# Kernel tuning notes

Measured on AMD Instinct MI355X. Metric: run time of the kernel, lower is better.

The kernel has to match this reference:

```python
import jax, jax.numpy as jnp
import numpy as np

N_NODES = 100000
N_EDGES = 640000
H = 128


def setup_inputs() -> dict:
    key = jax.random.key(0)
    ks = jax.random.split(key, 6)
    s = 1.0 / np.sqrt(H)
    x = jax.random.normal(ks[0], (N_NODES, H), dtype=jnp.float32)
    src = jax.random.randint(ks[1], (N_EDGES,), 0, N_NODES, dtype=jnp.int64)
    dst = jax.random.randint(ks[2], (N_EDGES,), 0, N_NODES, dtype=jnp.int64)
    W1 = jax.random.normal(ks[3], (H, H), dtype=jnp.float32) * s
    W2 = jax.random.normal(ks[4], (H, H), dtype=jnp.float32) * s
    W3 = jax.random.normal(ks[5], (H, 1), dtype=jnp.float32) * s
    return {
        "x": x, "src": src, "dst": dst,
        "W1": W1, "b1": jnp.zeros((H,), jnp.float32),
        "W2": W2, "b2": jnp.zeros((H,), jnp.float32),
        "W3": W3, "b3": jnp.zeros((1,), jnp.float32),
    }


def reference(x, src, dst, W1, b1, W2, b2, W3, b3):
    # per-edge gather of src/dst node feats, elementwise product: [E, H]
    h = x[src] * x[dst]
    # 3-layer MLP (Linear-ReLU-Linear-ReLU-Linear) per edge -> [E, 1]
    h = jax.nn.relu(h @ W1 + b1)
    h = jax.nn.relu(h @ W2 + b2)
    return h @ W3 + b3
```

## Files before the change

### kernel.cpp

```cpp
#include <hip/hip_runtime.h>
#include <hip/hip_bf16.h>

#define HDIM 128

typedef short bf16x8 __attribute__((ext_vector_type(8)));
typedef float f32x4 __attribute__((ext_vector_type(4)));

__device__ __forceinline__ short f2bf(float f) {
    __hip_bfloat16 h = __float2bfloat16(f);
    return __builtin_bit_cast(short, h);
}

__device__ __forceinline__ float bf2f(short s) {
    unsigned u = ((unsigned)(unsigned short)s) << 16;
    return __builtin_bit_cast(float, u);
}

__device__ __forceinline__ bf16x8 ldB(const short* sW, int n, int chunk) {
    return *(const bf16x8*)(sW + n * HDIM + ((chunk ^ (n & 7)) << 3));
}

__device__ __forceinline__ bf16x8 gatherA_f32(const float* xs, const float* xd, int k0) {
    float4 a0 = *(const float4*)(xs + k0);
    float4 a1 = *(const float4*)(xs + k0 + 4);
    float4 c0 = *(const float4*)(xd + k0);
    float4 c1 = *(const float4*)(xd + k0 + 4);
    bf16x8 r = { f2bf(a0.x * c0.x), f2bf(a0.y * c0.y), f2bf(a0.z * c0.z), f2bf(a0.w * c0.w),
                 f2bf(a1.x * c1.x), f2bf(a1.y * c1.y), f2bf(a1.z * c1.z), f2bf(a1.w * c1.w) };
    return r;
}

__global__ void cvt_kernel(const float* __restrict__ x, unsigned short* __restrict__ xb, int n4) {
    int i = blockIdx.x * blockDim.x + threadIdx.x;
    const int stride = gridDim.x * blockDim.x;
    for (; i < n4; i += stride) {
        float4 v = ((const float4*)x)[i];
        ushort4 o;
        o.x = (unsigned short)f2bf(v.x);
        o.y = (unsigned short)f2bf(v.y);
        o.z = (unsigned short)f2bf(v.z);
        o.w = (unsigned short)f2bf(v.w);
        ((ushort4*)xb)[i] = o;
    }
}

template<bool XBF>
__global__ __launch_bounds__(256, 2)
void edge_mlp_kernel(const float* __restrict__ x,
                     const unsigned short* __restrict__ xb,
                     const int* __restrict__ src,
                     const int* __restrict__ dst,
                     const float* __restrict__ W1, const float* __restrict__ b1,
                     const float* __restrict__ W2, const float* __restrict__ b2,
                     const float* __restrict__ W3, const float* __restrict__ b3,
                     float* __restrict__ out, int E, int ntiles)
{
    __shared__ short sW1[HDIM * HDIM];
    __shared__ short sW2[HDIM * HDIM];
    __shared__ short sH1[4][32 * 64];

    const int tid = threadIdx.x;

    {
        const int n  = tid & 127;
        const int kh = tid >> 7;
        for (int c = 0; c < 8; ++c) {
            const int kc = kh * 8 + c;
            const int k0 = kc * 8;
            short v1[8], v2[8];
            #pragma unroll
            for (int j = 0; j < 8; ++j) {
                v1[j] = f2bf(W1[(k0 + j) * HDIM + n]);
                v2[j] = f2bf(W2[(k0 + j) * HDIM + n]);
            }
            const int off = n * HDIM + ((kc ^ (n & 7)) << 3);
            bf16x8 t1 = { v1[0], v1[1], v1[2], v1[3], v1[4], v1[5], v1[6], v1[7] };
            bf16x8 t2 = { v2[0], v2[1], v2[2], v2[3], v2[4], v2[5], v2[6], v2[7] };
            *(bf16x8*)(sW1 + off) = t1;
            *(bf16x8*)(sW2 + off) = t2;
        }
    }
    __syncthreads();

    const int w    = tid >> 6;
    const int lane = tid & 63;
    const int g    = lane >> 4;
    const int e16  = lane & 15;
    short* myH1 = &sH1[w][0];

    float b1v[8], b2v[8], w3v[8];
    #pragma unroll
    for (int nt = 0; nt < 8; ++nt) {
        b1v[nt] = b1[nt * 16 + e16];
        b2v[nt] = b2[nt * 16 + e16];
        w3v[nt] = W3[nt * 16 + e16];
    }
    const float b3s = b3[0];

    if (blockIdx.x >= ntiles) return;

    int tile = blockIdx.x;
    int s0, d0, s1, d1;
    {
        const int base = (tile << 7) + (w << 5);
        int a0 = base + e16;       a0 = a0 < E ? a0 : 0;
        int a1 = base + 16 + e16;  a1 = a1 < E ? a1 : 0;
        s0 = src[a0]; d0 = dst[a0]; s1 = src[a1]; d1 = dst[a1];
    }
    bf16x8 rS0[4], rD0[4], rS1[4], rD1[4];
    if constexpr (XBF) {
        const unsigned short* pxs0 = xb + (size_t)s0 * HDIM;
        const unsigned short* pxd0 = xb + (size_t)d0 * HDIM;
        const unsigned short* pxs1 = xb + (size_t)s1 * HDIM;
        const unsigned short* pxd1 = xb + (size_t)d1 * HDIM;
        #pragma unroll
        for (int t = 0; t < 4; ++t) {
            const int k0 = t * 32 + g * 8;
            rS0[t] = *(const bf16x8*)(pxs0 + k0);
            rD0[t] = *(const bf16x8*)(pxd0 + k0);
            rS1[t] = *(const bf16x8*)(pxs1 + k0);
            rD1[t] = *(const bf16x8*)(pxd1 + k0);
        }
    }

    for (;;) {
        const int nxt = tile + gridDim.x;
        const bool hasNext = nxt < ntiles;

        int ns0, nd0, ns1, nd1;
        {
            const int nb = hasNext ? (nxt << 7) + (w << 5) : 0;
            int a0 = nb + e16;       a0 = a0 < E ? a0 : 0;
            int a1 = nb + 16 + e16;  a1 = a1 < E ? a1 : 0;
            ns0 = src[a0]; nd0 = dst[a0]; ns1 = src[a1]; nd1 = dst[a1];
        }

        const int base = (tile << 7) + (w << 5);

        f32x4 acc[2][8];
        #pragma unroll
        for (int nt = 0; nt < 8; ++nt) {
            f32x4 iv = { b1v[nt], b1v[nt], b1v[nt], b1v[nt] };
            acc[0][nt] = iv;
            acc[1][nt] = iv;
        }

        if constexpr (XBF) {
            #pragma unroll
            for (int t = 0; t < 4; ++t) {
                bf16x8 a0, a1;
                #pragma unroll
                for (int j = 0; j < 8; ++j) {
                    a0[j] = f2bf(bf2f(rS0[t][j]) * bf2f(rD0[t][j]));
                    a1[j] = f2bf(bf2f(rS1[t][j]) * bf2f(rD1[t][j]));
                }
                #pragma unroll
                for (int nt = 0; nt < 8; ++nt) {
                    bf16x8 bb = ldB(sW1, nt * 16 + e16, t * 4 + g);
                    acc[0][nt] = __builtin_amdgcn_mfma_f32_16x16x32_bf16(a0, bb, acc[0][nt], 0, 0, 0);
                    acc[1][nt] = __builtin_amdgcn_mfma_f32_16x16x32_bf16(a1, bb, acc[1][nt], 0, 0, 0);
                }
            }
        } else {
            const float* xs0 = x + (size_t)s0 * HDIM;
            const float* xd0 = x + (size_t)d0 * HDIM;
            const float* xs1 = x + (size_t)s1 * HDIM;
            const float* xd1 = x + (size_t)d1 * HDIM;
            #pragma unroll
            for (int t = 0; t < 4; ++t) {
                const int k0 = t * 32 + g * 8;
                bf16x8 a0 = gatherA_f32(xs0, xd0, k0);
                bf16x8 a1 = gatherA_f32(xs1, xd1, k0);
                #pragma unroll
                for (int nt = 0; nt < 8; ++nt) {
                    bf16x8 bb = ldB(sW1, nt * 16 + e16, t * 4 + g);
                    acc[0][nt] = __builtin_amdgcn_mfma_f32_16x16x32_bf16(a0, bb, acc[0][nt], 0, 0, 0);
                    acc[1][nt] = __builtin_amdgcn_mfma_f32_16x16x32_bf16(a1, bb, acc[1][nt], 0, 0, 0);
                }
            }
        }

        bf16x8 nS0[4], nD0[4], nS1[4], nD1[4];
        if constexpr (XBF) {
            const unsigned short* pxs0 = xb + (size_t)ns0 * HDIM;
            const unsigned short* pxd0 = xb + (size_t)nd0 * HDIM;
            const unsigned short* pxs1 = xb + (size_t)ns1 * HDIM;
            const unsigned short* pxd1 = xb + (size_t)nd1 * HDIM;
            #pragma unroll
            for (int t = 0; t < 4; ++t) {
                const int k0 = t * 32 + g * 8;
                nS0[t] = *(const bf16x8*)(pxs0 + k0);
                nD0[t] = *(const bf16x8*)(pxd0 + k0);
                nS1[t] = *(const bf16x8*)(pxs1 + k0);
                nD1[t] = *(const bf16x8*)(pxd1 + k0);
            }
        }

        f32x4 acc2[2][8];
        #pragma unroll
        for (int nt = 0; nt < 8; ++nt) {
            f32x4 iv = { b2v[nt], b2v[nt], b2v[nt], b2v[nt] };
            acc2[0][nt] = iv;
            acc2[1][nt] = iv;
        }
        #pragma unroll
        for (int khf = 0; khf < 2; ++khf) {
            #pragma unroll
            for (int ntl = 0; ntl < 4; ++ntl) {
                const int nt = khf * 4 + ntl;
                #pragma unroll
                for (int mt = 0; mt < 2; ++mt) {
                    #pragma unroll
                    for (int r = 0; r < 4; ++r) {
                        const int e  = mt * 16 + g * 4 + r;
                        const int kk = ntl * 16 + e16;
                        float v = acc[mt][nt][r];
                        v = v > 0.0f ? v : 0.0f;
                        myH1[e * 64 + (((kk >> 3) ^ (e & 7)) << 3) + (kk & 7)] = f2bf(v);
                    }
                }
            }
            #pragma unroll
            for (int tl = 0; tl < 2; ++tl) {
                const int ck = tl * 4 + g;
                bf16x8 a0 = *(const bf16x8*)(myH1 + e16 * 64 + ((ck ^ (e16 & 7)) << 3));
                bf16x8 a1 = *(const bf16x8*)(myH1 + (e16 + 16) * 64 + ((ck ^ ((e16 + 16) & 7)) << 3));
                const int t2 = khf * 2 + tl;
                #pragma unroll
                for (int nt = 0; nt < 8; ++nt) {
                    bf16x8 bb = ldB(sW2, nt * 16 + e16, t2 * 4 + g);
                    acc2[0][nt] = __builtin_amdgcn_mfma_f32_16x16x32_bf16(a0, bb, acc2[0][nt], 0, 0, 0);
                    acc2[1][nt] = __builtin_amdgcn_mfma_f32_16x16x32_bf16(a1, bb, acc2[1][nt], 0, 0, 0);
                }
            }
        }

        #pragma unroll
        for (int mt = 0; mt < 2; ++mt) {
            float p0 = 0.f, p1 = 0.f, p2 = 0.f, p3 = 0.f;
            #pragma unroll
            for (int nt = 0; nt < 8; ++nt) {
                f32x4 v = acc2[mt][nt];
                float r0 = v[0] > 0.f ? v[0] : 0.f;
                float r1 = v[1] > 0.f ? v[1] : 0.f;
                float r2 = v[2] > 0.f ? v[2] : 0.f;
                float r3 = v[3] > 0.f ? v[3] : 0.f;
                p0 += r0 * w3v[nt];
                p1 += r1 * w3v[nt];
                p2 += r2 * w3v[nt];
                p3 += r3 * w3v[nt];
            }
            #pragma unroll
            for (int off = 1; off < 16; off <<= 1) {
                p0 += __shfl_xor(p0, off);
                p1 += __shfl_xor(p1, off);
                p2 += __shfl_xor(p2, off);
                p3 += __shfl_xor(p3, off);
            }
            if (e16 == 0) {
                const int eb = base + mt * 16 + g * 4;
                if (eb + 0 < E) out[eb + 0] = p0 + b3s;
                if (eb + 1 < E) out[eb + 1] = p1 + b3s;
                if (eb + 2 < E) out[eb + 2] = p2 + b3s;
                if (eb + 3 < E) out[eb + 3] = p3 + b3s;
            }
        }

        if (!hasNext) break;
        tile = nxt;
        s0 = ns0; d0 = nd0; s1 = ns1; d1 = nd1;
        if constexpr (XBF) {
            #pragma unroll
            for (int t = 0; t < 4; ++t) {
                rS0[t] = nS0[t]; rD0[t] = nD0[t];
                rS1[t] = nS1[t]; rD1[t] = nD1[t];
            }
        }
    }
}

extern "C" void kernel_launch(void* const* d_in, const int* in_sizes, int n_in,
                              void* d_out, int out_size, void* d_ws, size_t ws_size,
                              hipStream_t stream) {
    const float* x   = (const float*)d_in[0];
    const int*   src = (const int*)d_in[1];
    const int*   dst = (const int*)d_in[2];
    const float* W1  = (const float*)d_in[3];
    const float* b1  = (const float*)d_in[4];
    const float* W2  = (const float*)d_in[5];
    const float* b2  = (const float*)d_in[6];
    const float* W3  = (const float*)d_in[7];
    const float* b3  = (const float*)d_in[8];
    float* out = (float*)d_out;

    const int xelems = in_sizes[0];
    const int E = in_sizes[1];
    const int ntiles = (E + 127) >> 7;
    const int grid = ntiles < 512 ? ntiles : 512;

    const size_t need = (size_t)xelems * sizeof(unsigned short);
    if (ws_size >= need) {
        unsigned short* xb = (unsigned short*)d_ws;
        const int n4 = xelems >> 2;
        hipLaunchKernelGGL(cvt_kernel, dim3(2048), dim3(256), 0, stream, x, xb, n4);
        hipLaunchKernelGGL((edge_mlp_kernel<true>), dim3(grid), dim3(256), 0, stream,
                           x, xb, src, dst, W1, b1, W2, b2, W3, b3, out, E, ntiles);
    } else {
        hipLaunchKernelGGL((edge_mlp_kernel<false>), dim3(grid), dim3(256), 0, stream,
                           x, (const unsigned short*)nullptr, src, dst,
                           W1, b1, W2, b2, W3, b3, out, E, ntiles);
    }
}
```

Measured before the change: 91.43 us.

## Bucket-sort edges by source node block to improve gather locality

```diff
diff --git a/kernel.cpp b/kernel.cpp
--- a/kernel.cpp
+++ b/kernel.cpp
@@ -2,6 +2,7 @@
 #include <hip/hip_bf16.h>
 
 #define HDIM 128
+#define NB   1024
 
 typedef short bf16x8 __attribute__((ext_vector_type(8)));
 typedef float f32x4 __attribute__((ext_vector_type(4)));
@@ -44,12 +45,53 @@
     }
 }
 
-template<bool XBF>
+__global__ void hist_kernel(const int* __restrict__ src, int* __restrict__ hist, int E) {
+    __shared__ int h[NB];
+    for (int i = threadIdx.x; i < NB; i += blockDim.x) h[i] = 0;
+    __syncthreads();
+    int i = blockIdx.x * blockDim.x + threadIdx.x;
+    for (; i < E; i += gridDim.x * blockDim.x) atomicAdd(&h[src[i] >> 7], 1);
+    __syncthreads();
+    for (int i2 = threadIdx.x; i2 < NB; i2 += blockDim.x)
+        if (h[i2]) atomicAdd(&hist[i2], h[i2]);
+}
+
+__global__ void scan_kernel(const int* __restrict__ hist, int* __restrict__ cursor) {
+    __shared__ int s[NB];
+    const int t = threadIdx.x;
+    int v = hist[t];
+    s[t] = v;
+    __syncthreads();
+    for (int off = 1; off < NB; off <<= 1) {
+        int add = (t >= off) ? s[t - off] : 0;
+        __syncthreads();
+        s[t] += add;
+        __syncthreads();
+    }
+    cursor[t] = s[t] - v;
+}
+
+__global__ void scatter_kernel(const int* __restrict__ src, const int* __restrict__ dst,
+                               int* __restrict__ cursor,
+                               int* __restrict__ ssrc, int* __restrict__ sdst,
+                               int* __restrict__ perm, int E) {
+    int i = blockIdx.x * blockDim.x + threadIdx.x;
+    for (; i < E; i += gridDim.x * blockDim.x) {
+        int sv = src[i];
+        int p = atomicAdd(&cursor[sv >> 7], 1);
+        ssrc[p] = sv;
+        sdst[p] = dst[i];
+        perm[p] = i;
+    }
+}
+
+template<int MODE>
 __global__ __launch_bounds__(256, 2)
 void edge_mlp_kernel(const float* __restrict__ x,
                      const unsigned short* __restrict__ xb,
-                     const int* __restrict__ src,
-                     const int* __restrict__ dst,
+                     const int* __restrict__ ssrc,
+                     const int* __restrict__ sdst,
+                     const int* __restrict__ perm,
                      const float* __restrict__ W1, const float* __restrict__ b1,
                      const float* __restrict__ W2, const float* __restrict__ b2,
                      const float* __restrict__ W3, const float* __restrict__ b3,
@@ -97,18 +139,29 @@
     }
     const float b3s = b3[0];
 
-    if (blockIdx.x >= ntiles) return;
-
-    int tile = blockIdx.x;
+    int t0, t1e, tstep;
+    if constexpr (MODE == 2) {
+        const int tp = (ntiles + gridDim.x - 1) / gridDim.x;
+        t0 = blockIdx.x * tp;
+        t1e = t0 + tp < ntiles ? t0 + tp : ntiles;
+        tstep = 1;
+    } else {
+        t0 = blockIdx.x;
+        t1e = ntiles;
+        tstep = gridDim.x;
+    }
+    if (t0 >= t1e) return;
+
+    int tile = t0;
     int s0, d0, s1, d1;
     {
         const int base = (tile << 7) + (w << 5);
         int a0 = base + e16;       a0 = a0 < E ? a0 : 0;
         int a1 = base + 16 + e16;  a1 = a1 < E ? a1 : 0;
-        s0 = src[a0]; d0 = dst[a0]; s1 = src[a1]; d1 = dst[a1];
+        s0 = ssrc[a0]; d0 = sdst[a0]; s1 = ssrc[a1]; d1 = sdst[a1];
     }
     bf16x8 rS0[4], rD0[4], rS1[4], rD1[4];
-    if constexpr (XBF) {
+    if constexpr (MODE >= 1) {
         const unsigned short* pxs0 = xb + (size_t)s0 * HDIM;
         const unsigned short* pxd0 = xb + (size_t)d0 * HDIM;
         const unsigned short* pxs1 = xb + (size_t)s1 * HDIM;
@@ -124,15 +177,15 @@
     }
 
     for (;;) {
-        const int nxt = tile + gridDim.x;
-        const bool hasNext = nxt < ntiles;
+        const int nxt = tile + tstep;
+        const bool hasNext = nxt < t1e;
 
         int ns0, nd0, ns1, nd1;
         {
             const int nb = hasNext ? (nxt << 7) + (w << 5) : 0;
             int a0 = nb + e16;       a0 = a0 < E ? a0 : 0;
             int a1 = nb + 16 + e16;  a1 = a1 < E ? a1 : 0;
-            ns0 = src[a0]; nd0 = dst[a0]; ns1 = src[a1]; nd1 = dst[a1];
+            ns0 = ssrc[a0]; nd0 = sdst[a0]; ns1 = ssrc[a1]; nd1 = sdst[a1];
         }
 
         const int base = (tile << 7) + (w << 5);
@@ -145,7 +198,7 @@
             acc[1][nt] = iv;
         }
 
-        if constexpr (XBF) {
+        if constexpr (MODE >= 1) {
             #pragma unroll
             for (int t = 0; t < 4; ++t) {
                 bf16x8 a0, a1;
@@ -181,7 +234,7 @@
         }
 
         bf16x8 nS0[4], nD0[4], nS1[4], nD1[4];
-        if constexpr (XBF) {
+        if constexpr (MODE >= 1) {
             const unsigned short* pxs0 = xb + (size_t)ns0 * HDIM;
             const unsigned short* pxd0 = xb + (size_t)nd0 * HDIM;
             const unsigned short* pxs1 = xb + (size_t)ns1 * HDIM;
@@ -259,17 +312,21 @@
             }
             if (e16 == 0) {
                 const int eb = base + mt * 16 + g * 4;
-                if (eb + 0 < E) out[eb + 0] = p0 + b3s;
-                if (eb + 1 < E) out[eb + 1] = p1 + b3s;
-                if (eb + 2 < E) out[eb + 2] = p2 + b3s;
-                if (eb + 3 < E) out[eb + 3] = p3 + b3s;
+                float pv[4] = { p0, p1, p2, p3 };
+                #pragma unroll
+                for (int j = 0; j < 4; ++j) {
+                    if (eb + j < E) {
+                        if constexpr (MODE == 2) out[perm[eb + j]] = pv[j] + b3s;
+                        else                     out[eb + j]       = pv[j] + b3s;
+                    }
+                }
             }
         }
 
         if (!hasNext) break;
         tile = nxt;
         s0 = ns0; d0 = nd0; s1 = ns1; d1 = nd1;
-        if constexpr (XBF) {
+        if constexpr (MODE >= 1) {
             #pragma unroll
             for (int t = 0; t < 4; ++t) {
                 rS0[t] = nS0[t]; rD0[t] = nD0[t];
@@ -278,6 +335,8 @@
         }
     }
 }
+
+static inline size_t align256(size_t v) { return (v + 255) & ~(size_t)255; }
 
 extern "C" void kernel_launch(void* const* d_in, const int* in_sizes, int n_in,
                               void* d_out, int out_size, void* d_ws, size_t ws_size,
@@ -298,16 +357,39 @@
     const int ntiles = (E + 127) >> 7;
     const int grid = ntiles < 512 ? ntiles : 512;
 
-    const size_t need = (size_t)xelems * sizeof(unsigned short);
-    if (ws_size >= need) {
+    const size_t xb_bytes  = (size_t)xelems * 2;
+    const size_t off_ssrc  = align256(xb_bytes);
+    const size_t off_sdst  = off_ssrc + (size_t)E * 4;
+    const size_t off_perm  = off_sdst + (size_t)E * 4;
+    const size_t off_cur   = align256(off_perm + (size_t)E * 4);
+    const size_t off_hist  = off_cur + NB * 4;
+    const size_t need_sort = off_hist + NB * 4;
+
+    if (ws_size >= need_sort) {
         unsigned short* xb = (unsigned short*)d_ws;
-        const int n4 = xelems >> 2;
-        hipLaunchKernelGGL(cvt_kernel, dim3(2048), dim3(256), 0, stream, x, xb, n4);
-        hipLaunchKernelGGL((edge_mlp_kernel<true>), dim3(grid), dim3(256), 0, stream,
-                           x, xb, src, dst, W1, b1, W2, b2, W3, b3, out, E, ntiles);
+        int* ssrc   = (int*)((char*)d_ws + off_ssrc);
+        int* sdst   = (int*)((char*)d_ws + off_sdst);
+        int* perm   = (int*)((char*)d_ws + off_perm);
+        int* cursor = (int*)((char*)d_ws + off_cur);
+        int* hist   = (int*)((char*)d_ws + off_hist);
+
+        hipMemsetAsync((char*)d_ws + off_cur, 0, 2 * NB * 4, stream);
+        hipLaunchKernelGGL(hist_kernel, dim3(512), dim3(256), 0, stream, src, hist, E);
+        hipLaunchKernelGGL(scan_kernel, dim3(1), dim3(NB), 0, stream, hist, cursor);
+        hipLaunchKernelGGL(scatter_kernel, dim3(1024), dim3(256), 0, stream,
+                           src, dst, cursor, ssrc, sdst, perm, E);
+        hipLaunchKernelGGL(cvt_kernel, dim3(2048), dim3(256), 0, stream, x, xb, xelems >> 2);
+        hipLaunchKernelGGL((edge_mlp_kernel<2>), dim3(grid), dim3(256), 0, stream,
+                           x, xb, ssrc, sdst, perm, W1, b1, W2, b2, W3, b3, out, E, ntiles);
+    } else if (ws_size >= xb_bytes) {
+        unsigned short* xb = (unsigned short*)d_ws;
+        hipLaunchKernelGGL(cvt_kernel, dim3(2048), dim3(256), 0, stream, x, xb, xelems >> 2);
+        hipLaunchKernelGGL((edge_mlp_kernel<1>), dim3(grid), dim3(256), 0, stream,
+                           x, xb, src, dst, (const int*)nullptr,
+                           W1, b1, W2, b2, W3, b3, out, E, ntiles);
     } else {
-        hipLaunchKernelGGL((edge_mlp_kernel<false>), dim3(grid), dim3(256), 0, stream,
-                           x, (const unsigned short*)nullptr, src, dst,
+        hipLaunchKernelGGL((edge_mlp_kernel<0>), dim3(grid), dim3(256), 0, stream,
+                           x, (const unsigned short*)nullptr, src, dst, (const int*)nullptr,
                            W1, b1, W2, b2, W3, b3, out, E, ntiles);
     }
 }
```

Result: slower. 279.1 us (+205.2%).
